# Kernel optimization log

Measured on AMD Instinct MI355X. Metric: run time of the kernel, lower is better.

## Reference

```python
import jax, jax.numpy as jnp
import numpy as np

N_EMBD = 768
N_HEAD = 12
HEAD_DIM = N_EMBD // N_HEAD
HIDDEN = 4 * N_EMBD
B, T = 4, 2048
EPS = 1e-5


def setup_inputs() -> dict:
    key = jax.random.key(0)
    ks = jax.random.split(key, 7)
    s = lambda fan_in: 1.0 / np.sqrt(fan_in)
    return {
        "x": jax.random.normal(ks[0], (B, T, N_EMBD), dtype=jnp.float32),
        "ln1_g": jnp.ones((N_EMBD,), jnp.float32),
        "ln1_b": jnp.zeros((N_EMBD,), jnp.float32),
        "W_attn": jax.random.normal(ks[1], (N_EMBD, 3 * N_EMBD), jnp.float32) * s(N_EMBD),
        "W_o": jax.random.normal(ks[2], (N_EMBD, N_EMBD), jnp.float32) * s(N_EMBD),
        "ln2_g": jnp.ones((N_EMBD,), jnp.float32),
        "ln2_b": jnp.zeros((N_EMBD,), jnp.float32),
        "W_fc": jax.random.normal(ks[3], (N_EMBD, HIDDEN), jnp.float32) * s(N_EMBD),
        "W_proj": jax.random.normal(ks[4], (HIDDEN, N_EMBD), jnp.float32) * s(HIDDEN),
    }


def _layernorm(x, g, b):
    mu = jnp.mean(x, axis=-1, keepdims=True)
    var = jnp.mean(jnp.square(x - mu), axis=-1, keepdims=True)
    return (x - mu) * jax.lax.rsqrt(var + EPS) * g + b


def _attention(x, W_attn, W_o):
    b, t, c = x.shape
    qkv = x @ W_attn  # [B,T,3C]
    q, k, v = jnp.split(qkv, 3, axis=-1)
    # [B,H,T,D]
    q = q.reshape(b, t, N_HEAD, HEAD_DIM).transpose(0, 2, 1, 3)
    k = k.reshape(b, t, N_HEAD, HEAD_DIM).transpose(0, 2, 1, 3)
    v = v.reshape(b, t, N_HEAD, HEAD_DIM).transpose(0, 2, 1, 3)
    scale = 1.0 / jnp.sqrt(jnp.float32(HEAD_DIM))
    att = jnp.einsum("bhqd,bhkd->bhqk", q, k) * scale  # [B,H,T,T]
    causal = jnp.arange(t)[:, None] >= jnp.arange(t)[None, :]
    att = jnp.where(causal, att, -jnp.inf)
    att = jax.nn.softmax(att, axis=-1)
    y = jnp.einsum("bhqk,bhkd->bhqd", att, v)
    y = y.transpose(0, 2, 1, 3).reshape(b, t, c)
    return y @ W_o


def reference(x, ln1_g, ln1_b, W_attn, W_o, ln2_g, ln2_b, W_fc, W_proj):
    x = x + _attention(_layernorm(x, ln1_g, ln1_b), W_attn, W_o)
    h = _layernorm(x, ln2_g, ln2_b)
    h = jax.nn.gelu(h @ W_fc, approximate=False) @ W_proj  # torch nn.GELU() is exact erf gelu
    return x + h
```

## Files before the change

### kernel.cpp

```cpp
#include <hip/hip_runtime.h>
#include <cstdint>
#include <cstddef>

#define B_ 4
#define T_ 2048
#define C_ 768
#define H_ 12
#define D_ 64
#define M_ (B_*T_)
#define C3_ 2304
#define HID_ 3072

typedef unsigned short ushort_t;
typedef __bf16 bf16x8_t __attribute__((ext_vector_type(8)));
typedef float f32x4 __attribute__((ext_vector_type(4)));

typedef const __attribute__((address_space(1))) void* gas_ptr;
typedef __attribute__((address_space(3))) void* las_ptr;

__device__ __forceinline__ void gload_lds16(const ushort_t* g, ushort_t* l) {
  __builtin_amdgcn_global_load_lds((gas_ptr)g, (las_ptr)l, 16, 0, 0);
}

__device__ __forceinline__ float bf2f(ushort_t h) {
  union { unsigned int u; float f; } cv; cv.u = ((unsigned int)h) << 16; return cv.f;
}
__device__ __forceinline__ ushort_t f2bf(float f) {
  union { float f; unsigned int u; } cv; cv.f = f;
  unsigned int u = cv.u;
  unsigned int r = (u + 0x7FFFu + ((u >> 16) & 1u)) >> 16;
  return (ushort_t)r;
}
__device__ __forceinline__ ushort_t f2bf_trunc(float f) {
  union { float f; unsigned int u; } cv; cv.f = f;
  return (ushort_t)(cv.u >> 16);
}

__device__ __forceinline__ float gelu_f(float v) {
  float z = fabsf(v) * 0.70710678118654752f;
  float t = __builtin_amdgcn_rcpf(fmaf(0.3275911f, z, 1.0f));
  float e = exp2f(z * z * -1.44269504088896340736f);
  float p = t * fmaf(t, fmaf(t, fmaf(t, fmaf(t, 1.061405429f, -1.453152027f),
                                     1.421413741f), -0.284496736f), 0.254829592f);
  float ea = fmaf(-p, e, 1.0f);
  float er = copysignf(ea, v);
  return 0.5f * v * (1.0f + er);
}

__global__ __launch_bounds__(256) void transpose_k(const float* __restrict__ in,
                                                   ushort_t* __restrict__ out, int K, int N) {
  __shared__ ushort_t tile[32][33];
  int nx = threadIdx.x, ky = threadIdx.y;
  int n0 = blockIdx.x * 32, k0 = blockIdx.y * 32;
#pragma unroll
  for (int i = 0; i < 4; i++)
    tile[ky + i * 8][nx] = f2bf(in[(size_t)(k0 + ky + i * 8) * N + n0 + nx]);
  __syncthreads();
#pragma unroll
  for (int i = 0; i < 4; i++)
    out[(size_t)(n0 + ky + i * 8) * K + k0 + nx] = tile[nx][ky + i * 8];
}

__global__ __launch_bounds__(256) void vtrans_k(const ushort_t* __restrict__ qkv,
                                                ushort_t* __restrict__ vg) {
  __shared__ ushort_t tile[32][33];
  int nx = threadIdx.x, ky = threadIdx.y;
  int t0 = blockIdx.x * 32, d0 = blockIdx.y * 32;
  int bh = blockIdx.z;
  int b = bh / H_, h = bh % H_;
  const ushort_t* src = qkv + (size_t)b * T_ * C3_ + 2 * C_ + h * D_;
#pragma unroll
  for (int i = 0; i < 4; i++)
    tile[ky + i * 8][nx] = src[(size_t)(t0 + ky + i * 8) * C3_ + d0 + nx];
  __syncthreads();
  ushort_t* dst = vg + (size_t)bh * D_ * T_;
#pragma unroll
  for (int i = 0; i < 4; i++)
    dst[(size_t)(d0 + ky + i * 8) * T_ + t0 + nx] = tile[nx][ky + i * 8];
}

__global__ __launch_bounds__(256) void ln_k(const float* __restrict__ x, const float* __restrict__ g,
                                            const float* __restrict__ bb, ushort_t* __restrict__ out) {
  __shared__ float red[8];
  int row = blockIdx.x, t = threadIdx.x;
  const float* xr = x + (size_t)row * C_;
  float v0 = xr[t], v1 = xr[t + 256], v2 = xr[t + 512];
  float s = v0 + v1 + v2;
  float s2 = v0 * v0 + v1 * v1 + v2 * v2;
#pragma unroll
  for (int m = 32; m >= 1; m >>= 1) { s += __shfl_xor(s, m); s2 += __shfl_xor(s2, m); }
  int w = t >> 6;
  if ((t & 63) == 0) { red[w * 2] = s; red[w * 2 + 1] = s2; }
  __syncthreads();
  s = red[0] + red[2] + red[4] + red[6];
  s2 = red[1] + red[3] + red[5] + red[7];
  float mu = s * (1.f / C_);
  float var = s2 * (1.f / C_) - mu * mu;
  float rstd = rsqrtf(var + 1e-5f);
  out[(size_t)row * C_ + t]       = f2bf((v0 - mu) * rstd * g[t] + bb[t]);
  out[(size_t)row * C_ + t + 256] = f2bf((v1 - mu) * rstd * g[t + 256] + bb[t + 256]);
  out[(size_t)row * C_ + t + 512] = f2bf((v2 - mu) * rstd * g[t + 512] + bb[t + 512]);
}

#define MFMA16(d, a, b) d = __builtin_amdgcn_mfma_f32_16x16x32_bf16(a, b, d, 0, 0, 0)

template <int EPI>
__global__ void gemm_bt_k(const ushort_t* __restrict__ A,
                          const ushort_t* __restrict__ Bt,
                          const float* __restrict__ res,
                          void* __restrict__ outp,
                          int N, int K) {
  __shared__ __align__(16) ushort_t As[2][128][32];
  __shared__ __align__(16) ushort_t Bs[2][128][32];
  int t = threadIdx.x;

  int nwg = (int)(gridDim.x * gridDim.y);
  int orig = (int)(blockIdx.y * gridDim.x + blockIdx.x);
  int swz = (nwg & 7) ? orig : ((orig & 7) * (nwg >> 3) + (orig >> 3));
  int bx = swz % (int)gridDim.x, by = swz / (int)gridDim.x;
  int bn = bx * 128, bm = by * 128;

  int lane = t & 63, w = t >> 6;
  int wm = (w >> 1) * 64, wn = (w & 1) * 64;
  int lm = lane & 15;

  int lr = lane >> 2;
  int lc = (((lane & 3) ^ ((lane >> 3) & 3)) * 8);
  int cx = (((lane >> 4) ^ ((lane >> 1) & 3)) * 8);

  const ushort_t* ga0 = A  + (size_t)(bm + w * 16 + lr) * K + lc;
  const ushort_t* gb0 = Bt + (size_t)(bn + w * 16 + lr) * K + lc;
  const size_t kstep64 = (size_t)64 * K;

  const f32x4 fz = {0.f, 0.f, 0.f, 0.f};
  f32x4 acc00 = fz, acc01 = fz, acc02 = fz, acc03 = fz;
  f32x4 acc10 = fz, acc11 = fz, acc12 = fz, acc13 = fz;
  f32x4 acc20 = fz, acc21 = fz, acc22 = fz, acc23 = fz;
  f32x4 acc30 = fz, acc31 = fz, acc32 = fz, acc33 = fz;

#define STAGE(BUF, KOFF) do {                                   \
    gload_lds16(ga0 + (KOFF), &As[BUF][w * 16][0]);             \
    gload_lds16(ga0 + kstep64 + (KOFF), &As[BUF][w * 16 + 64][0]); \
    gload_lds16(gb0 + (KOFF), &Bs[BUF][w * 16][0]);             \
    gload_lds16(gb0 + kstep64 + (KOFF), &Bs[BUF][w * 16 + 64][0]); \
  } while (0)

#define COMPUTE(BUF) do {                                            \
    bf16x8_t af0 = *(const bf16x8_t*)&As[BUF][wm + lm][cx];          \
    bf16x8_t af1 = *(const bf16x8_t*)&As[BUF][wm + 16 + lm][cx];     \
    bf16x8_t af2 = *(const bf16x8_t*)&As[BUF][wm + 32 + lm][cx];     \
    bf16x8_t af3 = *(const bf16x8_t*)&As[BUF][wm + 48 + lm][cx];     \
    bf16x8_t bg0 = *(const bf16x8_t*)&Bs[BUF][wn + lm][cx];          \
    bf16x8_t bg1 = *(const bf16x8_t*)&Bs[BUF][wn + 16 + lm][cx];     \
    bf16x8_t bg2 = *(const bf16x8_t*)&Bs[BUF][wn + 32 + lm][cx];     \
    bf16x8_t bg3 = *(const bf16x8_t*)&Bs[BUF][wn + 48 + lm][cx];     \
    MFMA16(acc00, af0, bg0); MFMA16(acc01, af0, bg1); MFMA16(acc02, af0, bg2); MFMA16(acc03, af0, bg3); \
    MFMA16(acc10, af1, bg0); MFMA16(acc11, af1, bg1); MFMA16(acc12, af1, bg2); MFMA16(acc13, af1, bg3); \
    MFMA16(acc20, af2, bg0); MFMA16(acc21, af2, bg1); MFMA16(acc22, af2, bg2); MFMA16(acc23, af2, bg3); \
    MFMA16(acc30, af3, bg0); MFMA16(acc31, af3, bg1); MFMA16(acc32, af3, bg2); MFMA16(acc33, af3, bg3); \
  } while (0)

  STAGE(0, 0);
  for (int k0 = 0; k0 < K; k0 += 64) {
    STAGE(1, k0 + 32);
    asm volatile("s_waitcnt vmcnt(4)" ::: "memory");
    __builtin_amdgcn_s_barrier();
    asm volatile("" ::: "memory");
    COMPUTE(0);
    asm volatile("" ::: "memory");
    __builtin_amdgcn_s_barrier();
    if (k0 + 64 < K) {
      STAGE(0, k0 + 64);
      asm volatile("s_waitcnt vmcnt(4)" ::: "memory");
    } else {
      asm volatile("s_waitcnt vmcnt(0)" ::: "memory");
    }
    __builtin_amdgcn_s_barrier();
    asm volatile("" ::: "memory");
    COMPUTE(1);
    asm volatile("" ::: "memory");
    __builtin_amdgcn_s_barrier();
  }
#undef STAGE
#undef COMPUTE

  int rowb = bm + wm + (lane >> 4) * 4;
  int colb = bn + wn + lm;

#define ST(vv, row, jj) do { \
    float v = (vv); \
    size_t idx = (size_t)(row) * N + colb + (jj) * 16; \
    if constexpr (EPI == 0) { ((ushort_t*)outp)[idx] = f2bf(v); } \
    else if constexpr (EPI == 1) { ((float*)outp)[idx] = v + res[idx]; } \
    else { ((ushort_t*)outp)[idx] = f2bf(gelu_f(v)); } \
  } while (0)
#define STROW(a0, a1, a2, a3, row, rr) \
    ST(a0[rr], row, 0); ST(a1[rr], row, 1); ST(a2[rr], row, 2); ST(a3[rr], row, 3);
#define STBLK(a0, a1, a2, a3, rbase) \
    STROW(a0, a1, a2, a3, (rbase), 0) STROW(a0, a1, a2, a3, (rbase) + 1, 1) \
    STROW(a0, a1, a2, a3, (rbase) + 2, 2) STROW(a0, a1, a2, a3, (rbase) + 3, 3)

  STBLK(acc00, acc01, acc02, acc03, rowb)
  STBLK(acc10, acc11, acc12, acc13, rowb + 16)
  STBLK(acc20, acc21, acc22, acc23, rowb + 32)
  STBLK(acc30, acc31, acc32, acc33, rowb + 48)
#undef ST
#undef STROW
#undef STBLK
}

template <int EPI>
__global__ __launch_bounds__(512, 2) void gemm256_k(const ushort_t* __restrict__ A,
                                                    const ushort_t* __restrict__ Bt,
                                                    void* __restrict__ outp,
                                                    int N, int K) {
  __shared__ __align__(16) ushort_t As[2][2][256][32];
  __shared__ __align__(16) ushort_t Bs[2][2][256][32];
  int t = threadIdx.x;
  int lane = t & 63, w = t >> 6;

  int nwg = (int)(gridDim.x * gridDim.y);
  int orig = (int)(blockIdx.y * gridDim.x + blockIdx.x);
  int swz = (nwg & 7) ? orig : ((orig & 7) * (nwg >> 3) + (orig >> 3));
  int bx = swz % (int)gridDim.x, by = swz / (int)gridDim.x;
  int bn = bx * 256, bm = by * 256;

  int wm = (w >> 2) * 128, wn = (w & 3) * 64;
  int lm = lane & 15, lq = lane >> 4;
  int pcx = (lq ^ ((lm >> 1) & 3)) * 8;

  int srow = w * 16 + (lane >> 2);
  int scol = (((lane & 3) ^ ((lane >> 3) & 3)) * 8);
  const ushort_t* gaS = A  + (size_t)(bm + srow) * K + scol;
  const ushort_t* gbS = Bt + (size_t)(bn + srow) * K + scol;
  const size_t rstep128 = (size_t)128 * K;

  f32x4 acc[8][4];
#pragma unroll
  for (int m = 0; m < 8; m++)
#pragma unroll
    for (int n = 0; n < 4; n++) acc[m][n] = {0.f, 0.f, 0.f, 0.f};

#define SA(BUF, TT, KH) do { int ko_ = (TT) * 64 + (KH) * 32;            \
    gload_lds16(gaS + ko_,            &As[BUF][KH][w * 16][0]);          \
    gload_lds16(gaS + rstep128 + ko_, &As[BUF][KH][128 + w * 16][0]);    \
  } while (0)
#define SB(BUF, TT, KH) do { int ko_ = (TT) * 64 + (KH) * 32;            \
    gload_lds16(gbS + ko_,            &Bs[BUF][KH][w * 16][0]);          \
    gload_lds16(gbS + rstep128 + ko_, &Bs[BUF][KH][128 + w * 16][0]);    \
  } while (0)

#define RDA(BUF, KH, MH)                                                      \
    af0 = *(const bf16x8_t*)&As[BUF][KH][wm + (MH) * 64 +  0 + lm][pcx];      \
    af1 = *(const bf16x8_t*)&As[BUF][KH][wm + (MH) * 64 + 16 + lm][pcx];      \
    af2 = *(const bf16x8_t*)&As[BUF][KH][wm + (MH) * 64 + 32 + lm][pcx];      \
    af3 = *(const bf16x8_t*)&As[BUF][KH][wm + (MH) * 64 + 48 + lm][pcx];
#define RDB(BUF, KH)                                                          \
    bg0 = *(const bf16x8_t*)&Bs[BUF][KH][wn +  0 + lm][pcx];                  \
    bg1 = *(const bf16x8_t*)&Bs[BUF][KH][wn + 16 + lm][pcx];                  \
    bg2 = *(const bf16x8_t*)&Bs[BUF][KH][wn + 32 + lm][pcx];                  \
    bg3 = *(const bf16x8_t*)&Bs[BUF][KH][wn + 48 + lm][pcx];

#define M4(MM, AF) MFMA16(acc[MM][0], AF, bg0); MFMA16(acc[MM][1], AF, bg1);  \
                   MFMA16(acc[MM][2], AF, bg2); MFMA16(acc[MM][3], AF, bg3);
#define MF(MB) M4((MB) + 0, af0) M4((MB) + 1, af1) M4((MB) + 2, af2) M4((MB) + 3, af3)

#define PH_MID do { asm volatile("" ::: "memory");                            \
    __builtin_amdgcn_s_barrier();                                             \
    asm volatile("s_waitcnt lgkmcnt(0)" ::: "memory");                        \
    __builtin_amdgcn_sched_barrier(0);                                        \
    __builtin_amdgcn_s_setprio(1); } while (0)
#define PH_BAR do { asm volatile("" ::: "memory");                            \
    __builtin_amdgcn_s_barrier(); } while (0)
#define VM8 asm volatile("s_waitcnt vmcnt(8)" ::: "memory")
#define VM4 asm volatile("s_waitcnt vmcnt(4)" ::: "memory")
#define VM0 asm volatile("s_waitcnt vmcnt(0)" ::: "memory")

  int NT = K >> 6;
  SA(0, 0, 0); SB(0, 0, 0); SA(0, 0, 1); SB(0, 0, 1); SA(1, 1, 0); SB(1, 1, 0);
  VM8;
  __builtin_amdgcn_s_barrier();

  for (int it = 0; it * 2 < NT; ++it) {
    int tt = it * 2;
    bool nl = (tt + 2 < NT);
    bf16x8_t af0, af1, af2, af3, bg0, bg1, bg2, bg3;

    RDA(0, 0, 0) RDB(0, 0) SA(1, tt + 1, 1);
    PH_MID; MF(0) __builtin_amdgcn_s_setprio(0); PH_BAR;
    RDA(0, 0, 1) RDB(0, 0) SB(1, tt + 1, 1);
    PH_MID; MF(4) __builtin_amdgcn_s_setprio(0); VM8; PH_BAR;
    RDA(0, 1, 0) RDB(0, 1) if (nl) SA(0, tt + 2, 0);
    PH_MID; MF(0) __builtin_amdgcn_s_setprio(0); PH_BAR;
    RDA(0, 1, 1) RDB(0, 1) if (nl) SB(0, tt + 2, 0);
    PH_MID; MF(4) __builtin_amdgcn_s_setprio(0);
    if (nl) { VM8; } else { VM4; }
    PH_BAR;
    RDA(1, 0, 0) RDB(1, 0) if (nl) SA(0, tt + 2, 1);
    PH_MID; MF(0) __builtin_amdgcn_s_setprio(0); PH_BAR;
    RDA(1, 0, 1) RDB(1, 0) if (nl) SB(0, tt + 2, 1);
    PH_MID; MF(4) __builtin_amdgcn_s_setprio(0);
    if (nl) { VM8; } else { VM0; }
    PH_BAR;
    RDA(1, 1, 0) RDB(1, 1) if (nl) SA(1, tt + 3, 0);
    PH_MID; MF(0) __builtin_amdgcn_s_setprio(0); PH_BAR;
    RDA(1, 1, 1) RDB(1, 1) if (nl) SB(1, tt + 3, 0);
    PH_MID; MF(4) __builtin_amdgcn_s_setprio(0);
    if (nl) { VM8; }
    PH_BAR;
  }
#undef SA
#undef SB
#undef RDA
#undef RDB
#undef M4
#undef MF
#undef PH_MID
#undef PH_BAR
#undef VM8
#undef VM4
#undef VM0

#pragma unroll
  for (int m = 0; m < 8; m++) {
    int row0 = bm + wm + m * 16 + lq * 4;
#pragma unroll
    for (int n = 0; n < 4; n++) {
      int col = bn + wn + n * 16 + lm;
#pragma unroll
      for (int r = 0; r < 4; r++) {
        float v = acc[m][n][r];
        size_t idx = (size_t)(row0 + r) * N + col;
        if constexpr (EPI == 0) ((ushort_t*)outp)[idx] = f2bf(v);
        else                    ((ushort_t*)outp)[idx] = f2bf(gelu_f(v));
      }
    }
  }
}

__device__ __forceinline__ void stage64(const ushort_t* __restrict__ g, size_t strideE,
                                        ushort_t* l, int w, int lane) {
  int rl = lane >> 3;
  int ce = ((lane & 7) ^ rl) << 3;
  const ushort_t* g0 = g + (size_t)(w * 16 + rl) * strideE + ce;
  gload_lds16(g0, l + (size_t)(w * 16) * 64);
  const ushort_t* g1 = g + (size_t)(w * 16 + 8 + rl) * strideE + ce;
  gload_lds16(g1, l + (size_t)(w * 16 + 8) * 64);
}

__global__ __launch_bounds__(256, 3) void attn_k(const ushort_t* __restrict__ qkv,
                                                 const ushort_t* __restrict__ vg,
                                                 ushort_t* __restrict__ y) {
  __shared__ __align__(16) ushort_t Ks[2][64][64];
  __shared__ __align__(16) ushort_t Vs[2][64][64];
  __shared__ __align__(16) ushort_t Ps[4][16][72];

  int t = threadIdx.x;
  int w = t >> 6, lane = t & 63;
  int lm = lane & 15, qq = lane >> 4, q8 = qq * 8;
  int bh = blockIdx.x;
  int qt = (int)gridDim.y - 1 - (int)blockIdx.y;
  int b = bh / H_, h = bh % H_;

  size_t baserow = (size_t)b * T_;
  const ushort_t* qkvb = qkv + baserow * C3_ + h * D_;
  const ushort_t* kbase = qkvb + C_;
  const ushort_t* vbase = vg + (size_t)bh * D_ * T_;

  int qrow0 = qt * 64 + w * 16;
  const ushort_t* qp = qkvb + (size_t)(qrow0 + lm) * C3_ + q8;
  bf16x8_t aq0 = *(const bf16x8_t*)(qp);
  bf16x8_t aq1 = *(const bf16x8_t*)(qp + 32);
  __builtin_amdgcn_s_waitcnt(0);

  const f32x4 fz = {0.f, 0.f, 0.f, 0.f};
  f32x4 aO0 = fz, aO1 = fz, aO2 = fz, aO3 = fz;
  f32x4 lsum = fz;

  const float SC = 0.125f * 1.44269504088896340736f;

#define BODY(CUR, KT, MASKED)                                                   \
  {                                                                             \
    const char* Kb = (const char*)&Ks[CUR][0][0];                               \
    const char* Vb = (const char*)&Vs[CUR][0][0];                               \
    const int rsw = (lm & 7) << 4;                                              \
    const int c0 = (qq * 16) ^ rsw;                                             \
    const int c1 = (64 + qq * 16) ^ rsw;                                        \
    bf16x8_t kf[8], vv[8];                                                      \
    _Pragma("unroll") for (int j = 0; j < 4; j++) {                             \
      int rb = (j * 16 + lm) << 7;                                              \
      kf[2*j]   = *(const bf16x8_t*)(Kb + rb + c0);                             \
      kf[2*j+1] = *(const bf16x8_t*)(Kb + rb + c1);                             \
      vv[2*j]   = *(const bf16x8_t*)(Vb + rb + c0);                             \
      vv[2*j+1] = *(const bf16x8_t*)(Vb + rb + c1);                             \
    }                                                                           \
    f32x4 sa0 = fz, sa1 = fz, sa2 = fz, sa3 = fz;                               \
    MFMA16(sa0, aq0, kf[0]); MFMA16(sa0, aq1, kf[1]);                           \
    MFMA16(sa1, aq0, kf[2]); MFMA16(sa1, aq1, kf[3]);                           \
    MFMA16(sa2, aq0, kf[4]); MFMA16(sa2, aq1, kf[5]);                           \
    MFMA16(sa3, aq0, kf[6]); MFMA16(sa3, aq1, kf[7]);                           \
    _Pragma("unroll") for (int j = 0; j < 4; j++) {                             \
      f32x4 sj = (j == 0) ? sa0 : (j == 1) ? sa1 : (j == 2) ? sa2 : sa3;        \
      _Pragma("unroll") for (int r2 = 0; r2 < 4; r2++) {                        \
        float v = sj[r2] * SC;                                                  \
        if (MASKED && (j * 16 + lm) > (w * 16 + qq * 4 + r2)) v = -1e30f;       \
        float p = exp2f(v);                                                     \
        lsum[r2] += p;                                                          \
        Ps[w][qq * 4 + r2][j * 16 + lm] = f2bf_trunc(p);                        \
      }                                                                         \
    }                                                                           \
    {                                                                           \
      bf16x8_t ap_lo = *(const bf16x8_t*)&Ps[w][lm][q8];                        \
      bf16x8_t ap_hi = *(const bf16x8_t*)&Ps[w][lm][32 + q8];                   \
      MFMA16(aO0, ap_lo, vv[0]); MFMA16(aO0, ap_hi, vv[1]);                     \
      MFMA16(aO1, ap_lo, vv[2]); MFMA16(aO1, ap_hi, vv[3]);                     \
      MFMA16(aO2, ap_lo, vv[4]); MFMA16(aO2, ap_hi, vv[5]);                     \
      MFMA16(aO3, ap_lo, vv[6]); MFMA16(aO3, ap_hi, vv[7]);                     \
    }                                                                           \
  }

  stage64(kbase, C3_, &Ks[0][0][0], w, lane);
  stage64(vbase, T_, &Vs[0][0][0], w, lane);
  int cur = 0;
  for (int kt = 0; kt <= qt; ++kt) {
    if (kt < qt) {
      stage64(kbase + (size_t)(kt + 1) * 64 * C3_, C3_, &Ks[cur ^ 1][0][0], w, lane);
      stage64(vbase + (size_t)(kt + 1) * 64,       T_,  &Vs[cur ^ 1][0][0], w, lane);
      asm volatile("s_waitcnt vmcnt(4)" ::: "memory");
    } else {
      asm volatile("s_waitcnt vmcnt(0)" ::: "memory");
    }
    __builtin_amdgcn_s_barrier();
    asm volatile("" ::: "memory");
    if (kt == qt) { BODY(cur, kt, true) }
    else          { BODY(cur, kt, false) }
    asm volatile("" ::: "memory");
    __builtin_amdgcn_s_barrier();
    cur ^= 1;
  }
#undef BODY

#pragma unroll
  for (int r2 = 0; r2 < 4; r2++) {
    float s = lsum[r2];
    s += __shfl_xor(s, 1);
    s += __shfl_xor(s, 2);
    s += __shfl_xor(s, 4);
    s += __shfl_xor(s, 8);
    float inv = 1.f / s;
    size_t orow = (baserow + qrow0 + qq * 4 + r2) * C_ + h * D_;
    y[orow + lm]      = f2bf(aO0[r2] * inv);
    y[orow + 16 + lm] = f2bf(aO1[r2] * inv);
    y[orow + 32 + lm] = f2bf(aO2[r2] * inv);
    y[orow + 48 + lm] = f2bf(aO3[r2] * inv);
  }
}

extern "C" void kernel_launch(void* const* d_in, const int* in_sizes, int n_in,
                              void* d_out, int out_size, void* d_ws, size_t ws_size,
                              hipStream_t stream) {
  (void)in_sizes; (void)n_in; (void)out_size; (void)ws_size;
  const float* x      = (const float*)d_in[0];
  const float* ln1_g  = (const float*)d_in[1];
  const float* ln1_b  = (const float*)d_in[2];
  const float* W_attn = (const float*)d_in[3];
  const float* W_o    = (const float*)d_in[4];
  const float* ln2_g  = (const float*)d_in[5];
  const float* ln2_b  = (const float*)d_in[6];
  const float* W_fc   = (const float*)d_in[7];
  const float* W_proj = (const float*)d_in[8];

  char* ws = (char*)d_ws;
  ushort_t* big  = (ushort_t*)(ws);
  ushort_t* Vg   = (ushort_t*)(ws + 37748736);
  ushort_t* tmp  = (ushort_t*)(ws + 50331648);
  float*    x2   = (float*)   (ws + 62914560);
  ushort_t* Wat  = (ushort_t*)(ws + 88080384);
  ushort_t* Wot  = (ushort_t*)(ws + 91619328);
  ushort_t* Wfct = (ushort_t*)(ws + 92798976);
  ushort_t* Wpt  = (ushort_t*)(ws + 97517568);

  dim3 tb(32, 8);
  transpose_k<<<dim3(C3_ / 32, C_ / 32), tb, 0, stream>>>(W_attn, Wat, C_, C3_);
  transpose_k<<<dim3(C_ / 32, C_ / 32), tb, 0, stream>>>(W_o, Wot, C_, C_);
  transpose_k<<<dim3(HID_ / 32, C_ / 32), tb, 0, stream>>>(W_fc, Wfct, C_, HID_);
  transpose_k<<<dim3(C_ / 32, HID_ / 32), tb, 0, stream>>>(W_proj, Wpt, HID_, C_);

  ln_k<<<M_, 256, 0, stream>>>(x, ln1_g, ln1_b, tmp);
  gemm_bt_k<0><<<dim3(C3_ / 128, M_ / 128), 256, 0, stream>>>(tmp, Wat, nullptr, big, C3_, C_);
  vtrans_k<<<dim3(T_ / 32, D_ / 32, B_ * H_), tb, 0, stream>>>(big, Vg);
  attn_k<<<dim3(B_ * H_, T_ / 64), 256, 0, stream>>>(big, Vg, tmp);
  gemm_bt_k<1><<<dim3(C_ / 128, M_ / 128), 256, 0, stream>>>(tmp, Wot, x, x2, C_, C_);
  ln_k<<<M_, 256, 0, stream>>>(x2, ln2_g, ln2_b, tmp);
  gemm256_k<2><<<dim3(HID_ / 256, M_ / 256), 512, 0, stream>>>(tmp, Wfct, big, HID_, C_);
  gemm_bt_k<1><<<dim3(C_ / 128, M_ / 128), 256, 0, stream>>>(big, Wpt, x2, d_out, C_, HID_);
}
```

Measured before the change: 385.1 us.

## Replace LDS-staged GEMM with register-direct global loads double-buffered in registers

The 128x128 bf16 GEMM no longer stages A and B tiles through shared memory with global_load_lds and barriers. Each wave now loads its MFMA operand fragments straight from global memory into registers, double-buffered across two K-halves. This removes the LDS traffic and the workgroup barriers. In exchange, each wave re-reads operand data that neighbouring waves also read, which raises global/L2 traffic and register pressure, and the loads are 16-byte per-lane strided rows rather than coalesced tiles.

```diff
diff --git a/kernel.cpp b/kernel.cpp
--- a/kernel.cpp
+++ b/kernel.cpp
@@ -105,15 +105,12 @@
 #define MFMA16(d, a, b) d = __builtin_amdgcn_mfma_f32_16x16x32_bf16(a, b, d, 0, 0, 0)
 
 template <int EPI>
-__global__ void gemm_bt_k(const ushort_t* __restrict__ A,
-                          const ushort_t* __restrict__ Bt,
-                          const float* __restrict__ res,
-                          void* __restrict__ outp,
-                          int N, int K) {
-  __shared__ __align__(16) ushort_t As[2][128][32];
-  __shared__ __align__(16) ushort_t Bs[2][128][32];
+__global__ __launch_bounds__(256) void gemm_rs_k(const ushort_t* __restrict__ A,
+                                                 const ushort_t* __restrict__ Bt,
+                                                 const float* __restrict__ res,
+                                                 void* __restrict__ outp,
+                                                 int N, int K) {
   int t = threadIdx.x;
-
   int nwg = (int)(gridDim.x * gridDim.y);
   int orig = (int)(blockIdx.y * gridDim.x + blockIdx.x);
   int swz = (nwg & 7) ? orig : ((orig & 7) * (nwg >> 3) + (orig >> 3));
@@ -122,15 +119,11 @@
 
   int lane = t & 63, w = t >> 6;
   int wm = (w >> 1) * 64, wn = (w & 1) * 64;
-  int lm = lane & 15;
-
-  int lr = lane >> 2;
-  int lc = (((lane & 3) ^ ((lane >> 3) & 3)) * 8);
-  int cx = (((lane >> 4) ^ ((lane >> 1) & 3)) * 8);
-
-  const ushort_t* ga0 = A  + (size_t)(bm + w * 16 + lr) * K + lc;
-  const ushort_t* gb0 = Bt + (size_t)(bn + w * 16 + lr) * K + lc;
-  const size_t kstep64 = (size_t)64 * K;
+  int lm = lane & 15, q8 = (lane >> 4) * 8;
+
+  const ushort_t* a0 = A  + (size_t)(bm + wm + lm) * K + q8;
+  const ushort_t* b0 = Bt + (size_t)(bn + wn + lm) * K + q8;
+  const size_t r16 = (size_t)16 * K;
 
   const f32x4 fz = {0.f, 0.f, 0.f, 0.f};
   f32x4 acc00 = fz, acc01 = fz, acc02 = fz, acc03 = fz;
@@ -138,51 +131,36 @@
   f32x4 acc20 = fz, acc21 = fz, acc22 = fz, acc23 = fz;
   f32x4 acc30 = fz, acc31 = fz, acc32 = fz, acc33 = fz;
 
-#define STAGE(BUF, KOFF) do {                                   \
-    gload_lds16(ga0 + (KOFF), &As[BUF][w * 16][0]);             \
-    gload_lds16(ga0 + kstep64 + (KOFF), &As[BUF][w * 16 + 64][0]); \
-    gload_lds16(gb0 + (KOFF), &Bs[BUF][w * 16][0]);             \
-    gload_lds16(gb0 + kstep64 + (KOFF), &Bs[BUF][w * 16 + 64][0]); \
+  bf16x8_t ka0, ka1, ka2, ka3, kb0, kb1, kb2, kb3;
+  bf16x8_t la0, la1, la2, la3, lb0, lb1, lb2, lb3;
+
+#define LDBANK(A0, A1, A2, A3, B0, B1, B2, B3, KOFF) do {        \
+    A0 = *(const bf16x8_t*)(a0 + (KOFF));                        \
+    A1 = *(const bf16x8_t*)(a0 + r16 + (KOFF));                  \
+    A2 = *(const bf16x8_t*)(a0 + 2 * r16 + (KOFF));              \
+    A3 = *(const bf16x8_t*)(a0 + 3 * r16 + (KOFF));              \
+    B0 = *(const bf16x8_t*)(b0 + (KOFF));                        \
+    B1 = *(const bf16x8_t*)(b0 + r16 + (KOFF));                  \
+    B2 = *(const bf16x8_t*)(b0 + 2 * r16 + (KOFF));              \
+    B3 = *(const bf16x8_t*)(b0 + 3 * r16 + (KOFF));              \
   } while (0)
 
-#define COMPUTE(BUF) do {                                            \
-    bf16x8_t af0 = *(const bf16x8_t*)&As[BUF][wm + lm][cx];          \
-    bf16x8_t af1 = *(const bf16x8_t*)&As[BUF][wm + 16 + lm][cx];     \
-    bf16x8_t af2 = *(const bf16x8_t*)&As[BUF][wm + 32 + lm][cx];     \
-    bf16x8_t af3 = *(const bf16x8_t*)&As[BUF][wm + 48 + lm][cx];     \
-    bf16x8_t bg0 = *(const bf16x8_t*)&Bs[BUF][wn + lm][cx];          \
-    bf16x8_t bg1 = *(const bf16x8_t*)&Bs[BUF][wn + 16 + lm][cx];     \
-    bf16x8_t bg2 = *(const bf16x8_t*)&Bs[BUF][wn + 32 + lm][cx];     \
-    bf16x8_t bg3 = *(const bf16x8_t*)&Bs[BUF][wn + 48 + lm][cx];     \
-    MFMA16(acc00, af0, bg0); MFMA16(acc01, af0, bg1); MFMA16(acc02, af0, bg2); MFMA16(acc03, af0, bg3); \
-    MFMA16(acc10, af1, bg0); MFMA16(acc11, af1, bg1); MFMA16(acc12, af1, bg2); MFMA16(acc13, af1, bg3); \
-    MFMA16(acc20, af2, bg0); MFMA16(acc21, af2, bg1); MFMA16(acc22, af2, bg2); MFMA16(acc23, af2, bg3); \
-    MFMA16(acc30, af3, bg0); MFMA16(acc31, af3, bg1); MFMA16(acc32, af3, bg2); MFMA16(acc33, af3, bg3); \
+#define CMP(A0, A1, A2, A3, B0, B1, B2, B3) do {                                 \
+    MFMA16(acc00, A0, B0); MFMA16(acc01, A0, B1); MFMA16(acc02, A0, B2); MFMA16(acc03, A0, B3); \
+    MFMA16(acc10, A1, B0); MFMA16(acc11, A1, B1); MFMA16(acc12, A1, B2); MFMA16(acc13, A1, B3); \
+    MFMA16(acc20, A2, B0); MFMA16(acc21, A2, B1); MFMA16(acc22, A2, B2); MFMA16(acc23, A2, B3); \
+    MFMA16(acc30, A3, B0); MFMA16(acc31, A3, B1); MFMA16(acc32, A3, B2); MFMA16(acc33, A3, B3); \
   } while (0)
 
-  STAGE(0, 0);
+  LDBANK(ka0, ka1, ka2, ka3, kb0, kb1, kb2, kb3, 0);
   for (int k0 = 0; k0 < K; k0 += 64) {
-    STAGE(1, k0 + 32);
-    asm volatile("s_waitcnt vmcnt(4)" ::: "memory");
-    __builtin_amdgcn_s_barrier();
-    asm volatile("" ::: "memory");
-    COMPUTE(0);
-    asm volatile("" ::: "memory");
-    __builtin_amdgcn_s_barrier();
-    if (k0 + 64 < K) {
-      STAGE(0, k0 + 64);
-      asm volatile("s_waitcnt vmcnt(4)" ::: "memory");
-    } else {
-      asm volatile("s_waitcnt vmcnt(0)" ::: "memory");
-    }
-    __builtin_amdgcn_s_barrier();
-    asm volatile("" ::: "memory");
-    COMPUTE(1);
-    asm volatile("" ::: "memory");
-    __builtin_amdgcn_s_barrier();
-  }
-#undef STAGE
-#undef COMPUTE
+    LDBANK(la0, la1, la2, la3, lb0, lb1, lb2, lb3, k0 + 32);
+    CMP(ka0, ka1, ka2, ka3, kb0, kb1, kb2, kb3);
+    if (k0 + 64 < K) LDBANK(ka0, ka1, ka2, ka3, kb0, kb1, kb2, kb3, k0 + 64);
+    CMP(la0, la1, la2, la3, lb0, lb1, lb2, lb3);
+  }
+#undef LDBANK
+#undef CMP
 
   int rowb = bm + wm + (lane >> 4) * 4;
   int colb = bn + wn + lm;
@@ -487,11 +465,11 @@
   transpose_k<<<dim3(C_ / 32, HID_ / 32), tb, 0, stream>>>(W_proj, Wpt, HID_, C_);
 
   ln_k<<<M_, 256, 0, stream>>>(x, ln1_g, ln1_b, tmp);
-  gemm_bt_k<0><<<dim3(C3_ / 128, M_ / 128), 256, 0, stream>>>(tmp, Wat, nullptr, big, C3_, C_);
+  gemm_rs_k<0><<<dim3(C3_ / 128, M_ / 128), 256, 0, stream>>>(tmp, Wat, nullptr, big, C3_, C_);
   vtrans_k<<<dim3(T_ / 32, D_ / 32, B_ * H_), tb, 0, stream>>>(big, Vg);
   attn_k<<<dim3(B_ * H_, T_ / 64), 256, 0, stream>>>(big, Vg, tmp);
-  gemm_bt_k<1><<<dim3(C_ / 128, M_ / 128), 256, 0, stream>>>(tmp, Wot, x, x2, C_, C_);
+  gemm_rs_k<1><<<dim3(C_ / 128, M_ / 128), 256, 0, stream>>>(tmp, Wot, x, x2, C_, C_);
   ln_k<<<M_, 256, 0, stream>>>(x2, ln2_g, ln2_b, tmp);
   gemm256_k<2><<<dim3(HID_ / 256, M_ / 256), 512, 0, stream>>>(tmp, Wfct, big, HID_, C_);
-  gemm_bt_k<1><<<dim3(C_ / 128, M_ / 128), 256, 0, stream>>>(big, Wpt, x2, d_out, C_, HID_);
-}
+  gemm_rs_k<1><<<dim3(C_ / 128, M_ / 128), 256, 0, stream>>>(big, Wpt, x2, d_out, C_, HID_);
+}
```

Measured after the change: 602.1 us. 1.56x slower.
